# Kernel tuning notes

Hardware: AMD Instinct MI355X
Metric: run time of the kernel (lower is better)

## Reference

```python
import jax, jax.numpy as jnp
import numpy as np

N, E = 100000, 250000
SD, CD = 128, 768


def setup_inputs() -> dict:
    key = jax.random.key(0)
    ks = jax.random.split(key, 12)
    z = jax.random.normal(ks[0], (N, SD), dtype=jnp.float32)
    chemistry = jax.random.normal(ks[1], (N, CD), dtype=jnp.float32)
    edge = jax.random.randint(ks[2], (E, 2), 0, N, dtype=jnp.int64)
    smiles_mask = (jax.random.uniform(ks[3], (N,)) < 0.8).astype(jnp.float32)
    s = 1.0 / np.sqrt(SD)
    W1s = jax.random.uniform(ks[4], (SD, SD // 2), jnp.float32, -s, s)
    b1s = jax.random.uniform(ks[5], (SD // 2,), jnp.float32, -s, s)
    s2 = 1.0 / np.sqrt(SD // 2)
    W2s = jax.random.uniform(ks[6], (SD // 2, 1), jnp.float32, -s2, s2)
    b2s = jax.random.uniform(ks[7], (1,), jnp.float32, -s2, s2)
    c = 1.0 / np.sqrt(CD)
    W1c = jax.random.uniform(ks[8], (CD, CD // 4), jnp.float32, -c, c)
    b1c = jax.random.uniform(ks[9], (CD // 4,), jnp.float32, -c, c)
    c2 = 1.0 / np.sqrt(CD // 4)
    W2c = jax.random.uniform(ks[10], (CD // 4, 1), jnp.float32, -c2, c2)
    b2c = jax.random.uniform(ks[11], (1,), jnp.float32, -c2, c2)
    alpha = jnp.float32(0.1)
    return {"z": z, "chemistry": chemistry, "edge": edge, "smiles_mask": smiles_mask,
            "W1s": W1s, "b1s": b1s, "W2s": W2s, "b2s": b2s,
            "W1c": W1c, "b1c": b1c, "W2c": W2c, "b2c": b2c, "alpha": alpha}


def reference(z, chemistry, edge, smiles_mask, W1s, b1s, W2s, b2s,
              W1c, b1c, W2c, b2c, alpha):
    src, dst = edge[:, 0], edge[:, 1]
    # structural branch: gather, product, 2-layer MLP (dropout = eval identity)
    structural_prod = z[src] * z[dst]                      # [E, SD]
    h_s = jax.nn.relu(structural_prod @ W1s + b1s)         # [E, SD//2]
    score_structural = (h_s @ W2s + b2s)[:, 0]             # [E]
    # chemical branch
    chemical_prod = chemistry[src] * chemistry[dst]        # [E, CD]
    h_c = jax.nn.relu(chemical_prod @ W1c + b1c)           # [E, CD//4]
    score_chemical = (h_c @ W2c + b2c)[:, 0]               # [E]
    both_valid = smiles_mask[src] * smiles_mask[dst]       # [E]
    score_chemical = both_valid * score_chemical
    return score_structural + alpha * score_chemical
```

## Files before the change

### kernel.cpp

```cpp
#include <hip/hip_runtime.h>
#include <hip/hip_bf16.h>
#include <stdint.h>

#define N_NODES 100000
#define NE      250000
#define SDIM    128
#define CDIM    768
#define HS      64
#define HC      192
#define TILE_E  32
#define NBLK    ((NE + TILE_E - 1) / TILE_E)

#define CT2     32
#define NT2     ((NE + CT2 - 1) / CT2)
#define CBLK2   256

typedef __attribute__((ext_vector_type(8))) short bf16x8;
typedef __attribute__((ext_vector_type(4))) float f32x4;

static __device__ __forceinline__ uint16_t f2bf(float f) {
    union { __hip_bfloat16 h; uint16_t u; } cv;
    cv.h = __float2bfloat16(f);
    return cv.u;
}
static __device__ __forceinline__ float bf2f(uint16_t u) {
    union { float f; uint32_t i; } cv; cv.i = ((uint32_t)u) << 16; return cv.f;
}

__global__ void k_convert_w(const float* __restrict__ W1c, uint16_t* __restrict__ W1cT) {
    const int tid = blockIdx.x * 256 + threadIdx.x;
    const int stride = gridDim.x * 256;
    for (int i = tid; i < HC * CDIM; i += stride) {
        const int n = i / CDIM, k = i - n * CDIM;
        W1cT[i] = f2bf(W1c[k * HC + n]);
    }
}

__global__ __launch_bounds__(256, 3) void k_structural(
    const float* __restrict__ z, const int* __restrict__ edge,
    const float* __restrict__ W1s, const float* __restrict__ b1s,
    const float* __restrict__ W2s, const float* __restrict__ b2s,
    const float* __restrict__ smask, const float* __restrict__ alphap,
    float* __restrict__ out, float* __restrict__ valid)
{
    __shared__ float Wl[SDIM * HS];
    __shared__ float Pl[TILE_E * 132];

    const int t = threadIdx.x;
    const int e0 = blockIdx.x * TILE_E;

    {
        const float4* src = (const float4*)W1s;
        float4* dst = (float4*)Wl;
        for (int m = t; m < SDIM * HS / 4; m += 256) dst[m] = src[m];
    }
    {
        const int el = t >> 3, p = t & 7;
        const int e = e0 + el;
        if (e < NE) {
            const int s = edge[2 * e], d = edge[2 * e + 1];
            const float* rs = z + (long)s * SDIM;
            const float* rd = z + (long)d * SDIM;
            #pragma unroll
            for (int cc = 0; cc < 2; ++cc) {
                const int c = p + cc * 8;
                float4 s0 = *(const float4*)(rs + c * 8);
                float4 s1 = *(const float4*)(rs + c * 8 + 4);
                float4 d0 = *(const float4*)(rd + c * 8);
                float4 d1 = *(const float4*)(rd + c * 8 + 4);
                float4 r0 = {s0.x * d0.x, s0.y * d0.y, s0.z * d0.z, s0.w * d0.w};
                float4 r1 = {s1.x * d1.x, s1.y * d1.y, s1.z * d1.z, s1.w * d1.w};
                *(float4*)(&Pl[el * 132 + c * 8]) = r0;
                *(float4*)(&Pl[el * 132 + c * 8 + 4]) = r1;
            }
        }
    }
    __syncthreads();

    const int el = t >> 3, p = t & 7;
    float h[8] = {0, 0, 0, 0, 0, 0, 0, 0};
    const float4* Wl4 = (const float4*)Wl;
    #pragma unroll 4
    for (int k = 0; k < SDIM; ++k) {
        const float pv = Pl[el * 132 + k];
        float4 w0 = Wl4[k * 16 + p * 2];
        float4 w1 = Wl4[k * 16 + p * 2 + 1];
        h[0] += pv * w0.x; h[1] += pv * w0.y; h[2] += pv * w0.z; h[3] += pv * w0.w;
        h[4] += pv * w1.x; h[5] += pv * w1.y; h[6] += pv * w1.z; h[7] += pv * w1.w;
    }
    float partial = 0.f;
    #pragma unroll
    for (int j = 0; j < 8; ++j) {
        const int c = p * 8 + j;
        partial += fmaxf(h[j] + b1s[c], 0.f) * W2s[c];
    }
    partial += __shfl_xor(partial, 1);
    partial += __shfl_xor(partial, 2);
    partial += __shfl_xor(partial, 4);
    const int e = e0 + el;
    if (p == 0 && e < NE) {
        out[e] = partial + b2s[0];
        const int s = edge[2 * e], d = edge[2 * e + 1];
        valid[e] = alphap[0] * smask[s] * smask[d];
    }
}

static __device__ __forceinline__ void cvt_store_bf(uint16_t* Abuf, int el, int ch,
                                                    int4 vs, int4 vd) {
    union { int4 v; uint16_t u[8]; } a, b, r;
    a.v = vs; b.v = vd;
    #pragma unroll
    for (int q = 0; q < 8; ++q) r.u[q] = f2bf(bf2f(a.u[q]) * bf2f(b.u[q]));
    const int byte = el * 1536 + ((ch * 16) ^ ((el & 7) << 4));
    *(int4*)((char*)Abuf + byte) = r.v;
}
static __device__ __forceinline__ void zero_store(uint16_t* Abuf, int el, int ch) {
    const int byte = el * 1536 + ((ch * 16) ^ ((el & 7) << 4));
    int4 z = {0, 0, 0, 0};
    *(int4*)((char*)Abuf + byte) = z;
}
static __device__ __forceinline__ void stage_f32(uint16_t* Abuf, int el, int ch,
                                                 const float* rs, const float* rd) {
    float4 a0 = *(const float4*)(rs + ch * 8);
    float4 a1 = *(const float4*)(rs + ch * 8 + 4);
    float4 b0 = *(const float4*)(rd + ch * 8);
    float4 b1 = *(const float4*)(rd + ch * 8 + 4);
    union { int4 v; uint16_t u[8]; } r;
    r.u[0] = f2bf(a0.x * b0.x); r.u[1] = f2bf(a0.y * b0.y);
    r.u[2] = f2bf(a0.z * b0.z); r.u[3] = f2bf(a0.w * b0.w);
    r.u[4] = f2bf(a1.x * b1.x); r.u[5] = f2bf(a1.y * b1.y);
    r.u[6] = f2bf(a1.z * b1.z); r.u[7] = f2bf(a1.w * b1.w);
    const int byte = el * 1536 + ((ch * 16) ^ ((el & 7) << 4));
    *(int4*)((char*)Abuf + byte) = r.v;
}

template<bool BF16TAB>
__global__ __launch_bounds__(768, 3) void k_chem_v7(
    const void* __restrict__ chemv, const int* __restrict__ edge,
    const uint16_t* __restrict__ W1cT, const float* __restrict__ b1c,
    const float* __restrict__ W2c, const float* __restrict__ b2c,
    const float* __restrict__ valid, float* __restrict__ out)
{
    __shared__ uint16_t A[2][CT2 * CDIM];
    __shared__ float xchg[6][64][20];
    __shared__ float part[2][CT2][8];
    __shared__ int   ebuf[2][2 * CT2];

    const int t = threadIdx.x;
    const int w = t >> 6, lane = t & 63, lr = lane & 15, lg = lane >> 4;
    const int cg = w >> 1, kh = w & 1;
    const int b = blockIdx.x;

    const int t0 = b * 30 + (b < 133 ? b : 133);
    const int t1 = t0 + 30 + (b < 133 ? 1 : 0);

    const uint16_t* chemB = (const uint16_t*)chemv;
    const float*    chemF = (const float*)chemv;

    bf16x8 Breg[24];
    #pragma unroll
    for (int ct = 0; ct < 2; ++ct) {
        const uint16_t* Bp = W1cT + (long)(cg * 32 + ct * 16 + lr) * CDIM + kh * 384 + lg * 8;
        #pragma unroll
        for (int kc = 0; kc < 12; ++kc)
            Breg[ct * 12 + kc] = *(const bf16x8*)(Bp + kc * 32);
    }
    #pragma unroll
    for (int i = 0; i < 24; ++i) asm volatile("" : "+v"(Breg[i]));

    float b1v[2], w2v[2];
    #pragma unroll
    for (int ct = 0; ct < 2; ++ct) {
        b1v[ct] = b1c[cg * 32 + ct * 16 + lr];
        w2v[ct] = W2c[cg * 32 + ct * 16 + lr];
    }
    const float b2 = b2c[0];

    const int elb = t / 96;
    const int ch  = t % 96;

    #pragma unroll
    for (int q = 0; q < 4; ++q) {
        const int el = elb + 8 * q;
        const int e  = t0 * CT2 + el;
        const bool ok = (e < NE);
        const int ee = ok ? e : 0;
        const int si = edge[2 * ee], di = edge[2 * ee + 1];
        if constexpr (BF16TAB) {
            int4 vs = *(const int4*)(chemB + (long)si * CDIM + ch * 8);
            int4 vd = *(const int4*)(chemB + (long)di * CDIM + ch * 8);
            if (ok) cvt_store_bf(A[0], el, ch, vs, vd);
            else    zero_store(A[0], el, ch);
        } else {
            if (ok) stage_f32(A[0], el, ch, chemF + (long)si * CDIM, chemF + (long)di * CDIM);
            else    zero_store(A[0], el, ch);
        }
    }
    if (t < CT2) {
        const int e = (t0 + 1) * CT2 + t;
        const int ee = (e < NE) ? e : 0;
        int2 p2 = *(const int2*)(edge + 2 * ee);
        *(int2*)&ebuf[(t0 + 1) & 1][2 * t] = p2;
    }
    float vld_cur = 0.f, vld_next = 0.f;
    if (t < CT2) {
        const int e = t0 * CT2 + t;
        vld_next = (e < NE) ? valid[e] : 0.f;
    }
    __syncthreads();

    const int swz = (lr & 7) << 4;
    const int rb0 = lr * 1536;
    const int rb1 = rb0 + 16 * 1536;

    for (int ti = t0; ti < t1; ++ti) {
        const int it = ti - t0, cur = it & 1;
        const bool pf  = (ti + 1 < t1);
        const bool pf2 = (ti + 2 < t1);

        if (pf) {
            uint16_t* dst = A[cur ^ 1];
            const int ebase = (ti + 1) * CT2;
            const int par = (ti + 1) & 1;
            int2 e0p = *(const int2*)&ebuf[par][2 * elb];
            int2 e1p = *(const int2*)&ebuf[par][2 * (elb + 8)];
            int2 e2p = *(const int2*)&ebuf[par][2 * (elb + 16)];
            int2 e3p = *(const int2*)&ebuf[par][2 * (elb + 24)];
            if constexpr (BF16TAB) {
                {
                    int4 vs0 = *(const int4*)(chemB + (long)e0p.x * CDIM + ch * 8);
                    int4 vd0 = *(const int4*)(chemB + (long)e0p.y * CDIM + ch * 8);
                    int4 vs1 = *(const int4*)(chemB + (long)e1p.x * CDIM + ch * 8);
                    int4 vd1 = *(const int4*)(chemB + (long)e1p.y * CDIM + ch * 8);
                    if (ebase + elb < NE)     cvt_store_bf(dst, elb,     ch, vs0, vd0);
                    else                      zero_store(dst, elb, ch);
                    if (ebase + elb + 8 < NE) cvt_store_bf(dst, elb + 8, ch, vs1, vd1);
                    else                      zero_store(dst, elb + 8, ch);
                }
                {
                    int4 vs2 = *(const int4*)(chemB + (long)e2p.x * CDIM + ch * 8);
                    int4 vd2 = *(const int4*)(chemB + (long)e2p.y * CDIM + ch * 8);
                    int4 vs3 = *(const int4*)(chemB + (long)e3p.x * CDIM + ch * 8);
                    int4 vd3 = *(const int4*)(chemB + (long)e3p.y * CDIM + ch * 8);
                    if (ebase + elb + 16 < NE) cvt_store_bf(dst, elb + 16, ch, vs2, vd2);
                    else                       zero_store(dst, elb + 16, ch);
                    if (ebase + elb + 24 < NE) cvt_store_bf(dst, elb + 24, ch, vs3, vd3);
                    else                       zero_store(dst, elb + 24, ch);
                }
            } else {
                #pragma unroll
                for (int q = 0; q < 4; ++q) {
                    const int el = elb + 8 * q;
                    int2 ep = (q == 0) ? e0p : (q == 1) ? e1p : (q == 2) ? e2p : e3p;
                    if (ebase + el < NE)
                        stage_f32(dst, el, ch, chemF + (long)ep.x * CDIM,
                                  chemF + (long)ep.y * CDIM);
                    else zero_store(dst, el, ch);
                }
            }
        }
        if (pf2 && t < CT2) {
            const int e = (ti + 2) * CT2 + t;
            const int ee = (e < NE) ? e : 0;
            int2 p2 = *(const int2*)(edge + 2 * ee);
            *(int2*)&ebuf[ti & 1][2 * t] = p2;
        }

        if (ti > t0 && t < CT2) {
            const int e = (ti - 1) * CT2 + t;
            if (e < NE) {
                float s_ = 0.f;
                #pragma unroll
                for (int c6 = 0; c6 < 6; ++c6) s_ += part[cur ^ 1][t][c6];
                atomicAdd(&out[e], vld_cur * (s_ + b2));
            }
        }
        if (t < CT2) {
            vld_cur = vld_next;
            if (pf) {
                const int e = (ti + 1) * CT2 + t;
                vld_next = (e < NE) ? valid[e] : 0.f;
            }
        }

        f32x4 acc00 = {0,0,0,0}, acc01 = {0,0,0,0}, acc10 = {0,0,0,0}, acc11 = {0,0,0,0};
        {
            const char* Ab = (const char*)A[cur];
            #pragma unroll
            for (int kc = 0; kc < 12; ++kc) {
                const int off = ((kh * 12 + kc) * 64 + lg * 16) ^ swz;
                bf16x8 a0 = *(const bf16x8*)(Ab + rb0 + off);
                bf16x8 a1 = *(const bf16x8*)(Ab + rb1 + off);
                acc00 = __builtin_amdgcn_mfma_f32_16x16x32_bf16(a0, Breg[kc],      acc00, 0, 0, 0);
                acc10 = __builtin_amdgcn_mfma_f32_16x16x32_bf16(a1, Breg[kc],      acc10, 0, 0, 0);
                acc01 = __builtin_amdgcn_mfma_f32_16x16x32_bf16(a0, Breg[12 + kc], acc01, 0, 0, 0);
                acc11 = __builtin_amdgcn_mfma_f32_16x16x32_bf16(a1, Breg[12 + kc], acc11, 0, 0, 0);
            }
        }

        if (kh == 1) {
            float* xp = xchg[cg][lane];
            *(float4*)(xp +  0) = (float4){acc00[0], acc00[1], acc00[2], acc00[3]};
            *(float4*)(xp +  4) = (float4){acc01[0], acc01[1], acc01[2], acc01[3]};
            *(float4*)(xp +  8) = (float4){acc10[0], acc10[1], acc10[2], acc10[3]};
            *(float4*)(xp + 12) = (float4){acc11[0], acc11[1], acc11[2], acc11[3]};
        }
        __syncthreads();
        if (kh == 0) {
            const float* xp = xchg[cg][lane];
            float4 x0 = *(const float4*)(xp + 0);
            float4 x1 = *(const float4*)(xp + 4);
            float4 x2 = *(const float4*)(xp + 8);
            float4 x3 = *(const float4*)(xp + 12);
            acc00[0] += x0.x; acc00[1] += x0.y; acc00[2] += x0.z; acc00[3] += x0.w;
            acc01[0] += x1.x; acc01[1] += x1.y; acc01[2] += x1.z; acc01[3] += x1.w;
            acc10[0] += x2.x; acc10[1] += x2.y; acc10[2] += x2.z; acc10[3] += x2.w;
            acc11[0] += x3.x; acc11[1] += x3.y; acc11[2] += x3.z; acc11[3] += x3.w;
            #pragma unroll
            for (int r = 0; r < 4; ++r) {
                float p0 = fmaxf(acc00[r] + b1v[0], 0.f) * w2v[0]
                         + fmaxf(acc01[r] + b1v[1], 0.f) * w2v[1];
                float p1 = fmaxf(acc10[r] + b1v[0], 0.f) * w2v[0]
                         + fmaxf(acc11[r] + b1v[1], 0.f) * w2v[1];
                #pragma unroll
                for (int m = 1; m <= 8; m <<= 1) {
                    p0 += __shfl_xor(p0, m);
                    p1 += __shfl_xor(p1, m);
                }
                if (lr == 0) {
                    part[cur][lg * 4 + r][cg]      = p0;
                    part[cur][16 + lg * 4 + r][cg] = p1;
                }
            }
        }
        __syncthreads();
    }

    if (t < CT2) {
        const int e = (t1 - 1) * CT2 + t;
        if (e < NE) {
            const int cur = (t1 - 1 - t0) & 1;
            float s_ = 0.f;
            #pragma unroll
            for (int c6 = 0; c6 < 6; ++c6) s_ += part[cur][t][c6];
            atomicAdd(&out[e], vld_cur * (s_ + b2));
        }
    }
}

extern "C" void kernel_launch(void* const* d_in, const int* in_sizes, int n_in,
                              void* d_out, int out_size, void* d_ws, size_t ws_size,
                              hipStream_t stream)
{
    const float* z     = (const float*)d_in[0];
    const float* chem  = (const float*)d_in[1];
    const int*   edge  = (const int*)d_in[2];
    const float* smask = (const float*)d_in[3];
    const float* W1s   = (const float*)d_in[4];
    const float* b1s   = (const float*)d_in[5];
    const float* W2s   = (const float*)d_in[6];
    const float* b2s   = (const float*)d_in[7];
    const float* W1c   = (const float*)d_in[8];
    const float* b1c   = (const float*)d_in[9];
    const float* W2c   = (const float*)d_in[10];
    const float* b2c   = (const float*)d_in[11];
    const float* alpha = (const float*)d_in[12];
    float* out = (float*)d_out;

    uint16_t* W1cT = (uint16_t*)d_ws;
    float* valid = (float*)((char*)d_ws + (size_t)HC * CDIM * 2);

    k_convert_w<<<dim3(64), dim3(256), 0, stream>>>(W1c, W1cT);

    k_structural<<<dim3(NBLK), dim3(256), 0, stream>>>(
        z, edge, W1s, b1s, W2s, b2s, smask, alpha, out, valid);

    k_chem_v7<false><<<dim3(CBLK2), dim3(768), 0, stream>>>(
        (const void*)chem, edge, W1cT, b1c, W2c, b2c, valid, out);
}
```

Before: 329.7 us.

## Stage chemistry gathers via async global_load_lds and shrink edge tile to 16

Rewrites the chemical-branch kernel to gather raw fp32 chemistry rows directly into LDS with global_load_lds while the MFMA tile runs. After the matmul, the staged rows are multiplied and converted to bf16 into a single A buffer. The edge tile shrinks from 32 to 16 rows and each block now covers about 61 tiles, and the bounds checks are dropped because 250000 divides evenly by 16. The aim is to hide gather latency behind compute without holding the loaded values in registers. In exchange, the fp32 staging buffer needs about 98KB of LDS, which lowers occupancy, and halving the MFMA work per tile doubles the number of barriers.

```diff
diff --git a/kernel.cpp b/kernel.cpp
--- a/kernel.cpp
+++ b/kernel.cpp
@@ -11,9 +11,9 @@
 #define TILE_E  32
 #define NBLK    ((NE + TILE_E - 1) / TILE_E)
 
-#define CT2     32
-#define NT2     ((NE + CT2 - 1) / CT2)
-#define CBLK2   256
+#define CT3     16
+#define NT3     (NE / CT3)
+#define CBLK3   256
 
 typedef __attribute__((ext_vector_type(8))) short bf16x8;
 typedef __attribute__((ext_vector_type(4))) float f32x4;
@@ -23,8 +23,10 @@
     cv.h = __float2bfloat16(f);
     return cv.u;
 }
-static __device__ __forceinline__ float bf2f(uint16_t u) {
-    union { float f; uint32_t i; } cv; cv.i = ((uint32_t)u) << 16; return cv.f;
+static __device__ __forceinline__ void gload_lds16(const void* g, void* l) {
+    __builtin_amdgcn_global_load_lds(
+        (const __attribute__((address_space(1))) void*)g,
+        (__attribute__((address_space(3))) void*)l, 16, 0, 0);
 }
 
 __global__ void k_convert_w(const float* __restrict__ W1c, uint16_t* __restrict__ W1cT) {
@@ -105,20 +107,6 @@
     }
 }
 
-static __device__ __forceinline__ void cvt_store_bf(uint16_t* Abuf, int el, int ch,
-                                                    int4 vs, int4 vd) {
-    union { int4 v; uint16_t u[8]; } a, b, r;
-    a.v = vs; b.v = vd;
-    #pragma unroll
-    for (int q = 0; q < 8; ++q) r.u[q] = f2bf(bf2f(a.u[q]) * bf2f(b.u[q]));
-    const int byte = el * 1536 + ((ch * 16) ^ ((el & 7) << 4));
-    *(int4*)((char*)Abuf + byte) = r.v;
-}
-static __device__ __forceinline__ void zero_store(uint16_t* Abuf, int el, int ch) {
-    const int byte = el * 1536 + ((ch * 16) ^ ((el & 7) << 4));
-    int4 z = {0, 0, 0, 0};
-    *(int4*)((char*)Abuf + byte) = z;
-}
 static __device__ __forceinline__ void stage_f32(uint16_t* Abuf, int el, int ch,
                                                  const float* rs, const float* rd) {
     float4 a0 = *(const float4*)(rs + ch * 8);
@@ -134,28 +122,25 @@
     *(int4*)((char*)Abuf + byte) = r.v;
 }
 
-template<bool BF16TAB>
-__global__ __launch_bounds__(768, 3) void k_chem_v7(
-    const void* __restrict__ chemv, const int* __restrict__ edge,
+__global__ __launch_bounds__(768, 3) void k_chem_v9(
+    const float* __restrict__ chemF, const int* __restrict__ edge,
     const uint16_t* __restrict__ W1cT, const float* __restrict__ b1c,
     const float* __restrict__ W2c, const float* __restrict__ b2c,
     const float* __restrict__ valid, float* __restrict__ out)
 {
-    __shared__ uint16_t A[2][CT2 * CDIM];
-    __shared__ float xchg[6][64][20];
-    __shared__ float part[2][CT2][8];
-    __shared__ int   ebuf[2][2 * CT2];
+    __shared__ float    raw[CT3 * 2 * CDIM];
+    __shared__ uint16_t A[CT3 * CDIM];
+    __shared__ float    xchg[6][64][12];
+    __shared__ float    part[2][CT3][8];
+    __shared__ int      ebuf[2][2 * CT3];
 
     const int t = threadIdx.x;
     const int w = t >> 6, lane = t & 63, lr = lane & 15, lg = lane >> 4;
     const int cg = w >> 1, kh = w & 1;
     const int b = blockIdx.x;
 
-    const int t0 = b * 30 + (b < 133 ? b : 133);
-    const int t1 = t0 + 30 + (b < 133 ? 1 : 0);
-
-    const uint16_t* chemB = (const uint16_t*)chemv;
-    const float*    chemF = (const float*)chemv;
+    const int t0 = b * 61 + (b < 9 ? b : 9);
+    const int t1 = t0 + 61 + (b < 9 ? 1 : 0);
 
     bf16x8 Breg[24];
     #pragma unroll
@@ -176,175 +161,127 @@
     }
     const float b2 = b2c[0];
 
-    const int elb = t / 96;
-    const int ch  = t % 96;
-
-    #pragma unroll
-    for (int q = 0; q < 4; ++q) {
-        const int el = elb + 8 * q;
-        const int e  = t0 * CT2 + el;
-        const bool ok = (e < NE);
-        const int ee = ok ? e : 0;
-        const int si = edge[2 * ee], di = edge[2 * ee + 1];
-        if constexpr (BF16TAB) {
-            int4 vs = *(const int4*)(chemB + (long)si * CDIM + ch * 8);
-            int4 vd = *(const int4*)(chemB + (long)di * CDIM + ch * 8);
-            if (ok) cvt_store_bf(A[0], el, ch, vs, vd);
-            else    zero_store(A[0], el, ch);
-        } else {
-            if (ok) stage_f32(A[0], el, ch, chemF + (long)si * CDIM, chemF + (long)di * CDIM);
-            else    zero_store(A[0], el, ch);
-        }
-    }
-    if (t < CT2) {
-        const int e = (t0 + 1) * CT2 + t;
-        const int ee = (e < NE) ? e : 0;
-        int2 p2 = *(const int2*)(edge + 2 * ee);
-        *(int2*)&ebuf[(t0 + 1) & 1][2 * t] = p2;
+    int rj[8], offj[8];
+    #pragma unroll
+    for (int j = 0; j < 8; ++j) {
+        const int off = (w * 8 + j) * 1024 + lane * 16;
+        rj[j]   = off / 3072;
+        offj[j] = off - rj[j] * 3072;
+    }
+
+    #pragma unroll
+    for (int q = 0; q < 2; ++q) {
+        const int slot = t + q * 768;
+        const int el = slot / 96, ch = slot - (slot / 96) * 96;
+        const int e = t0 * CT3 + el;
+        const int si = edge[2 * e], di = edge[2 * e + 1];
+        stage_f32(A, el, ch, chemF + (long)si * CDIM, chemF + (long)di * CDIM);
+    }
+    if (t < 2 * CT3 && t0 + 1 < t1) {
+        const int e = (t0 + 1) * CT3 + (t >> 1);
+        ebuf[(t0 + 1) & 1][t] = edge[2 * e + (t & 1)];
     }
     float vld_cur = 0.f, vld_next = 0.f;
-    if (t < CT2) {
-        const int e = t0 * CT2 + t;
-        vld_next = (e < NE) ? valid[e] : 0.f;
-    }
+    if (t < CT3) vld_next = valid[t0 * CT3 + t];
     __syncthreads();
 
     const int swz = (lr & 7) << 4;
     const int rb0 = lr * 1536;
-    const int rb1 = rb0 + 16 * 1536;
 
     for (int ti = t0; ti < t1; ++ti) {
-        const int it = ti - t0, cur = it & 1;
+        const int cur = (ti - t0) & 1;
         const bool pf  = (ti + 1 < t1);
         const bool pf2 = (ti + 2 < t1);
 
         if (pf) {
-            uint16_t* dst = A[cur ^ 1];
-            const int ebase = (ti + 1) * CT2;
             const int par = (ti + 1) & 1;
-            int2 e0p = *(const int2*)&ebuf[par][2 * elb];
-            int2 e1p = *(const int2*)&ebuf[par][2 * (elb + 8)];
-            int2 e2p = *(const int2*)&ebuf[par][2 * (elb + 16)];
-            int2 e3p = *(const int2*)&ebuf[par][2 * (elb + 24)];
-            if constexpr (BF16TAB) {
-                {
-                    int4 vs0 = *(const int4*)(chemB + (long)e0p.x * CDIM + ch * 8);
-                    int4 vd0 = *(const int4*)(chemB + (long)e0p.y * CDIM + ch * 8);
-                    int4 vs1 = *(const int4*)(chemB + (long)e1p.x * CDIM + ch * 8);
-                    int4 vd1 = *(const int4*)(chemB + (long)e1p.y * CDIM + ch * 8);
-                    if (ebase + elb < NE)     cvt_store_bf(dst, elb,     ch, vs0, vd0);
-                    else                      zero_store(dst, elb, ch);
-                    if (ebase + elb + 8 < NE) cvt_store_bf(dst, elb + 8, ch, vs1, vd1);
-                    else                      zero_store(dst, elb + 8, ch);
-                }
-                {
-                    int4 vs2 = *(const int4*)(chemB + (long)e2p.x * CDIM + ch * 8);
-                    int4 vd2 = *(const int4*)(chemB + (long)e2p.y * CDIM + ch * 8);
-                    int4 vs3 = *(const int4*)(chemB + (long)e3p.x * CDIM + ch * 8);
-                    int4 vd3 = *(const int4*)(chemB + (long)e3p.y * CDIM + ch * 8);
-                    if (ebase + elb + 16 < NE) cvt_store_bf(dst, elb + 16, ch, vs2, vd2);
-                    else                       zero_store(dst, elb + 16, ch);
-                    if (ebase + elb + 24 < NE) cvt_store_bf(dst, elb + 24, ch, vs3, vd3);
-                    else                       zero_store(dst, elb + 24, ch);
-                }
-            } else {
-                #pragma unroll
-                for (int q = 0; q < 4; ++q) {
-                    const int el = elb + 8 * q;
-                    int2 ep = (q == 0) ? e0p : (q == 1) ? e1p : (q == 2) ? e2p : e3p;
-                    if (ebase + el < NE)
-                        stage_f32(dst, el, ch, chemF + (long)ep.x * CDIM,
-                                  chemF + (long)ep.y * CDIM);
-                    else zero_store(dst, el, ch);
-                }
-            }
-        }
-        if (pf2 && t < CT2) {
-            const int e = (ti + 2) * CT2 + t;
-            const int ee = (e < NE) ? e : 0;
-            int2 p2 = *(const int2*)(edge + 2 * ee);
-            *(int2*)&ebuf[ti & 1][2 * t] = p2;
-        }
-
-        if (ti > t0 && t < CT2) {
-            const int e = (ti - 1) * CT2 + t;
-            if (e < NE) {
-                float s_ = 0.f;
-                #pragma unroll
-                for (int c6 = 0; c6 < 6; ++c6) s_ += part[cur ^ 1][t][c6];
-                atomicAdd(&out[e], vld_cur * (s_ + b2));
-            }
-        }
-        if (t < CT2) {
+            #pragma unroll
+            for (int j = 0; j < 8; ++j) {
+                const int node = ebuf[par][rj[j]];
+                const char* g = (const char*)(chemF + (long)node * CDIM) + offj[j];
+                char* l = (char*)raw + (w * 8 + j) * 1024;
+                gload_lds16(g, l);
+            }
+        }
+
+        if (pf2 && t < 2 * CT3) {
+            const int e = (ti + 2) * CT3 + (t >> 1);
+            ebuf[ti & 1][t] = edge[2 * e + (t & 1)];
+        }
+
+        if (ti > t0 && t < CT3) {
+            const int e = (ti - 1) * CT3 + t;
+            float s_ = 0.f;
+            #pragma unroll
+            for (int c6 = 0; c6 < 6; ++c6) s_ += part[cur ^ 1][t][c6];
+            atomicAdd(&out[e], vld_cur * (s_ + b2));
+        }
+        if (t < CT3) {
             vld_cur = vld_next;
-            if (pf) {
-                const int e = (ti + 1) * CT2 + t;
-                vld_next = (e < NE) ? valid[e] : 0.f;
-            }
-        }
-
-        f32x4 acc00 = {0,0,0,0}, acc01 = {0,0,0,0}, acc10 = {0,0,0,0}, acc11 = {0,0,0,0};
+            if (pf) vld_next = valid[(ti + 1) * CT3 + t];
+        }
+
+        f32x4 acc0 = {0, 0, 0, 0}, acc1 = {0, 0, 0, 0};
         {
-            const char* Ab = (const char*)A[cur];
+            const char* Ab = (const char*)A;
             #pragma unroll
             for (int kc = 0; kc < 12; ++kc) {
                 const int off = ((kh * 12 + kc) * 64 + lg * 16) ^ swz;
                 bf16x8 a0 = *(const bf16x8*)(Ab + rb0 + off);
-                bf16x8 a1 = *(const bf16x8*)(Ab + rb1 + off);
-                acc00 = __builtin_amdgcn_mfma_f32_16x16x32_bf16(a0, Breg[kc],      acc00, 0, 0, 0);
-                acc10 = __builtin_amdgcn_mfma_f32_16x16x32_bf16(a1, Breg[kc],      acc10, 0, 0, 0);
-                acc01 = __builtin_amdgcn_mfma_f32_16x16x32_bf16(a0, Breg[12 + kc], acc01, 0, 0, 0);
-                acc11 = __builtin_amdgcn_mfma_f32_16x16x32_bf16(a1, Breg[12 + kc], acc11, 0, 0, 0);
+                acc0 = __builtin_amdgcn_mfma_f32_16x16x32_bf16(a0, Breg[kc],      acc0, 0, 0, 0);
+                acc1 = __builtin_amdgcn_mfma_f32_16x16x32_bf16(a0, Breg[12 + kc], acc1, 0, 0, 0);
             }
         }
 
         if (kh == 1) {
             float* xp = xchg[cg][lane];
-            *(float4*)(xp +  0) = (float4){acc00[0], acc00[1], acc00[2], acc00[3]};
-            *(float4*)(xp +  4) = (float4){acc01[0], acc01[1], acc01[2], acc01[3]};
-            *(float4*)(xp +  8) = (float4){acc10[0], acc10[1], acc10[2], acc10[3]};
-            *(float4*)(xp + 12) = (float4){acc11[0], acc11[1], acc11[2], acc11[3]};
+            *(float4*)(xp + 0) = (float4){acc0[0], acc0[1], acc0[2], acc0[3]};
+            *(float4*)(xp + 4) = (float4){acc1[0], acc1[1], acc1[2], acc1[3]};
         }
         __syncthreads();
+
         if (kh == 0) {
             const float* xp = xchg[cg][lane];
             float4 x0 = *(const float4*)(xp + 0);
             float4 x1 = *(const float4*)(xp + 4);
-            float4 x2 = *(const float4*)(xp + 8);
-            float4 x3 = *(const float4*)(xp + 12);
-            acc00[0] += x0.x; acc00[1] += x0.y; acc00[2] += x0.z; acc00[3] += x0.w;
-            acc01[0] += x1.x; acc01[1] += x1.y; acc01[2] += x1.z; acc01[3] += x1.w;
-            acc10[0] += x2.x; acc10[1] += x2.y; acc10[2] += x2.z; acc10[3] += x2.w;
-            acc11[0] += x3.x; acc11[1] += x3.y; acc11[2] += x3.z; acc11[3] += x3.w;
+            acc0[0] += x0.x; acc0[1] += x0.y; acc0[2] += x0.z; acc0[3] += x0.w;
+            acc1[0] += x1.x; acc1[1] += x1.y; acc1[2] += x1.z; acc1[3] += x1.w;
             #pragma unroll
             for (int r = 0; r < 4; ++r) {
-                float p0 = fmaxf(acc00[r] + b1v[0], 0.f) * w2v[0]
-                         + fmaxf(acc01[r] + b1v[1], 0.f) * w2v[1];
-                float p1 = fmaxf(acc10[r] + b1v[0], 0.f) * w2v[0]
-                         + fmaxf(acc11[r] + b1v[1], 0.f) * w2v[1];
+                float p0 = fmaxf(acc0[r] + b1v[0], 0.f) * w2v[0]
+                         + fmaxf(acc1[r] + b1v[1], 0.f) * w2v[1];
                 #pragma unroll
-                for (int m = 1; m <= 8; m <<= 1) {
-                    p0 += __shfl_xor(p0, m);
-                    p1 += __shfl_xor(p1, m);
-                }
-                if (lr == 0) {
-                    part[cur][lg * 4 + r][cg]      = p0;
-                    part[cur][16 + lg * 4 + r][cg] = p1;
-                }
+                for (int m = 1; m <= 8; m <<= 1) p0 += __shfl_xor(p0, m);
+                if (lr == 0) part[cur][lg * 4 + r][cg] = p0;
+            }
+        }
+
+        if (pf) {
+            #pragma unroll
+            for (int q = 0; q < 4; ++q) {
+                const int p = t + q * 768;
+                const int rp = p / 192;
+                const int j  = p - rp * 192;
+                const char* rawb = (const char*)raw + rp * 6144 + j * 16;
+                float4 s4 = *(const float4*)(rawb);
+                float4 d4 = *(const float4*)(rawb + 3072);
+                union { uint16_t u[4]; uint2 v; } r;
+                r.u[0] = f2bf(s4.x * d4.x); r.u[1] = f2bf(s4.y * d4.y);
+                r.u[2] = f2bf(s4.z * d4.z); r.u[3] = f2bf(s4.w * d4.w);
+                const int byte = rp * 1536 + ((j * 8) ^ ((rp & 7) << 4));
+                *(uint2*)((char*)A + byte) = r.v;
             }
         }
         __syncthreads();
     }
 
-    if (t < CT2) {
-        const int e = (t1 - 1) * CT2 + t;
-        if (e < NE) {
-            const int cur = (t1 - 1 - t0) & 1;
-            float s_ = 0.f;
-            #pragma unroll
-            for (int c6 = 0; c6 < 6; ++c6) s_ += part[cur][t][c6];
-            atomicAdd(&out[e], vld_cur * (s_ + b2));
-        }
+    if (t < CT3) {
+        const int e = (t1 - 1) * CT3 + t;
+        const int cur = (t1 - 1 - t0) & 1;
+        float s_ = 0.f;
+        #pragma unroll
+        for (int c6 = 0; c6 < 6; ++c6) s_ += part[cur][t][c6];
+        atomicAdd(&out[e], vld_cur * (s_ + b2));
     }
 }
 
@@ -375,6 +312,6 @@
     k_structural<<<dim3(NBLK), dim3(256), 0, stream>>>(
         z, edge, W1s, b1s, W2s, b2s, smask, alpha, out, valid);
 
-    k_chem_v7<false><<<dim3(CBLK2), dim3(768), 0, stream>>>(
-        (const void*)chem, edge, W1cT, b1c, W2c, b2c, valid, out);
-}
+    k_chem_v9<<<dim3(CBLK3), dim3(768), 0, stream>>>(
+        chem, edge, W1cT, b1c, W2c, b2c, valid, out);
+}
```

New measurement: 423.9 us. 28.6% more time.
